# Kernel tuning notes

Measured on AMD Instinct MI355X. Metric: run time of the kernel, lower is better.

The kernel has to match this reference:

```python
import jax, jax.numpy as jnp
import numpy as np

N_NODES = 100000
N_EDGES = 1600000
IN_C, HID_C, OUT_C = 128, 128, 64


def gcn_conv(x, src, dst, ew, W, b, n_nodes):
    """PyG GCNConv: symmetric-normalized aggregation with added self-loops.

    out = D^{-1/2} (A + I) D^{-1/2} (x @ W) + b,  D = deg(A+I)
    """
    h = x @ W  # [N, C_out]
    # degree at target nodes, including self-loop weight of 1
    deg = jax.ops.segment_sum(ew, dst, num_segments=n_nodes) + 1.0  # [N]
    dinv = jnp.where(deg > 0, jax.lax.rsqrt(deg), 0.0)
    norm = dinv[src] * ew * dinv[dst]  # [E]
    # gather-scale-scatter over edges + self-loop term (norm_ii = 1/deg_i)
    agg = jax.ops.segment_sum(h[src] * norm[:, None], dst, num_segments=n_nodes)
    agg = agg + h * (dinv * dinv)[:, None]
    return agg + b


def setup_inputs() -> dict:
    key = jax.random.key(0)
    ks = jax.random.split(key, 7)
    x = jax.random.normal(ks[0], (N_NODES, IN_C), dtype=jnp.float32)
    edge_index = jax.random.randint(ks[1], (2, N_EDGES), 0, N_NODES, dtype=jnp.int32)
    edge_weight = jax.random.uniform(ks[2], (N_EDGES,), dtype=jnp.float32)
    W1 = jax.random.normal(ks[3], (IN_C, HID_C), dtype=jnp.float32) / np.sqrt(IN_C)
    b1 = jnp.zeros((HID_C,), dtype=jnp.float32)
    W2 = jax.random.normal(ks[4], (HID_C, OUT_C), dtype=jnp.float32) / np.sqrt(HID_C)
    b2 = jnp.zeros((OUT_C,), dtype=jnp.float32)
    return {"x": x, "edge_index": edge_index, "edge_weight": edge_weight,
            "W1": W1, "b1": b1, "W2": W2, "b2": b2}


def reference(x, edge_index, edge_weight, W1, b1, W2, b2):
    src, dst = edge_index[0], edge_index[1]
    n = x.shape[0]
    h = gcn_conv(x, src, dst, edge_weight, W1, b1, n)
    h = jax.nn.relu(h)
    out = gcn_conv(h, src, dst, edge_weight, W2, b2, n)
    return out
```

## Files before the change

kernel.cpp:

```cpp
#include <hip/hip_runtime.h>


#define N_NODES 100000
#define CHUNK   2048
#define NBUCK   196
#define BSHIFT  9
#define BNODES  512
#define CAP     10240

typedef __attribute__((ext_vector_type(8))) short bf16x8;
typedef __attribute__((ext_vector_type(4))) float f32x4;

__device__ __forceinline__ unsigned bf16r(float f) {
    unsigned u = __float_as_uint(f);
    return (u + 0x7fffu + ((u >> 16) & 1u)) >> 16;
}
__device__ __forceinline__ float bf_lo(unsigned u) { return __uint_as_float(u << 16); }
__device__ __forceinline__ float bf_hi(unsigned u) { return __uint_as_float(u & 0xffff0000u); }


__global__ __launch_bounds__(256) void partA1_kernel(
    const int* __restrict__ dst, int* __restrict__ histmat, int E)
{
    __shared__ int hist[256];
    int t = threadIdx.x, blk = blockIdx.x;
    hist[t] = 0;
    __syncthreads();
    int e0 = blk * CHUNK;
    int nv = min(CHUNK, E - e0);
#pragma unroll
    for (int j = 0; j < CHUNK / 256; ++j) {
        int idx = t + j * 256;
        if (idx < nv) atomicAdd(&hist[dst[e0 + idx] >> BSHIFT], 1);
    }
    __syncthreads();
    histmat[blk * 256 + t] = hist[t];
}


__global__ __launch_bounds__(256) void scanB_kernel(
    int* __restrict__ histmat, int* __restrict__ bucketSize, int NBLK)
{
    __shared__ int sums[256];
    int b = blockIdx.x, t = threadIdx.x;
    const int PER = (NBLK + 255) / 256;
    int loc[8];
    int s = 0;
#pragma unroll 8
    for (int j = 0; j < PER; ++j) {
        int r = t * PER + j;
        int v = (r < NBLK) ? histmat[r * 256 + b] : 0;
        loc[j] = v; s += v;
    }
    sums[t] = s;
    __syncthreads();
    int v = s;
#pragma unroll
    for (int off = 1; off < 256; off <<= 1) {
        int a = (t >= off) ? sums[t - off] : 0;
        __syncthreads();
        sums[t] += a;
        __syncthreads();
    }
    if (t == 255) bucketSize[b] = sums[255];
    int run = sums[t] - v;
#pragma unroll 8
    for (int j = 0; j < PER; ++j) {
        int r = t * PER + j;
        if (r < NBLK) { histmat[r * 256 + b] = run; run += loc[j]; }
    }
}


__global__ __launch_bounds__(256) void partA2_kernel(
    const int* __restrict__ src, const int* __restrict__ dst,
    const float* __restrict__ ew, const int* __restrict__ histmat,
    uint2* __restrict__ csrTmp, int E)
{
    __shared__ int hist[256], sc[256], exc[256], lcur[256], basel[256];
    __shared__ uint2 ent[CHUNK];
    __shared__ unsigned short bof[CHUNK];

    int t = threadIdx.x, blk = blockIdx.x;
    hist[t] = 0; lcur[t] = 0;
    basel[t] = histmat[blk * 256 + t];
    __syncthreads();

    int e0 = blk * CHUNK;
    int nv = min(CHUNK, E - e0);
    int dv[CHUNK / 256]; int sv[CHUNK / 256]; unsigned wv[CHUNK / 256];
#pragma unroll
    for (int j = 0; j < CHUNK / 256; ++j) {
        int idx = t + j * 256;
        if (idx < nv) {
            int e = e0 + idx;
            dv[j] = dst[e]; sv[j] = src[e]; wv[j] = __float_as_uint(ew[e]);
            atomicAdd(&hist[dv[j] >> BSHIFT], 1);
        } else dv[j] = -1;
    }
    __syncthreads();
    int hv = hist[t];
    sc[t] = hv;
    __syncthreads();
#pragma unroll
    for (int off = 1; off < 256; off <<= 1) {
        int a = (t >= off) ? sc[t - off] : 0;
        __syncthreads();
        sc[t] += a;
        __syncthreads();
    }
    exc[t] = sc[t] - hv;
    __syncthreads();
#pragma unroll
    for (int j = 0; j < CHUNK / 256; ++j) {
        if (dv[j] >= 0) {
            int b  = dv[j] >> BSHIFT;
            int dl = dv[j] & (BNODES - 1);
            int p  = exc[b] + atomicAdd(&lcur[b], 1);
            ent[p] = make_uint2(((unsigned)dl << 17) | (unsigned)sv[j], wv[j]);
            bof[p] = (unsigned short)b;
        }
    }
    __syncthreads();
#pragma unroll
    for (int j = 0; j < CHUNK / 256; ++j) {
        int i = t + j * 256;
        if (i < nv) {
            int b = bof[i];
            size_t addr = (size_t)b * CAP + basel[b] + (i - exc[b]);
            csrTmp[addr] = ent[i];
        }
    }
}


__global__ __launch_bounds__(1024) void bucketB1_kernel(
    const uint2* __restrict__ csrTmp, const int* __restrict__ bucketSize,
    float* __restrict__ dinv, uint2* __restrict__ nodeinfo, int N)
{
    __shared__ unsigned long long dc[BNODES];
    __shared__ int scn[BNODES];
    int b = blockIdx.x, t = threadIdx.x;
    if (t < BNODES) dc[t] = 0ull;
    __syncthreads();

    int sz = bucketSize[b];
    const uint2* reg = csrTmp + (size_t)b * CAP;
    for (int i = t; i < sz; i += 1024) {
        uint2 en = reg[i];
        int dl = (int)(en.x >> 17);
        unsigned fx = (unsigned)__float2uint_rn(__uint_as_float(en.y) * 16777216.0f);
        atomicAdd(&dc[dl], (1ull << 32) | (unsigned long long)fx);
    }
    __syncthreads();

    int cnt = 0; float dv = 1.0f;
    if (t < BNODES) {
        unsigned long long v = dc[t];
        cnt = (int)(v >> 32);
        float deg = (float)(unsigned)(v & 0xffffffffull) * (1.0f / 16777216.0f);
        dv = rsqrtf(deg + 1.0f);
        scn[t] = cnt;
    }
    __syncthreads();
#pragma unroll
    for (int off = 1; off < BNODES; off <<= 1) {
        int a = 0;
        if (t < BNODES && t >= off) a = scn[t - off];
        __syncthreads();
        if (t < BNODES) scn[t] += a;
        __syncthreads();
    }
    if (t < BNODES) {
        int excl = scn[t] - cnt;
        int gn = b * BNODES + t;
        if (gn < N) {
            dinv[gn] = dv;
            nodeinfo[gn] = make_uint2((unsigned)(b * CAP + excl), (unsigned)cnt);
        }
    }
}


__global__ __launch_bounds__(1024) void bucketB2_kernel(
    const uint2* __restrict__ csrTmp, const int* __restrict__ bucketSize,
    const uint2* __restrict__ nodeinfo, const float* __restrict__ dinv,
    uint2* __restrict__ csrF, int N)
{
    __shared__ float dinv_l[BNODES];
    __shared__ int beg[BNODES], cur[BNODES];
    int b = blockIdx.x, t = threadIdx.x;
    if (t < BNODES) {
        int gn = b * BNODES + t;
        float dv = 1.0f; int bg = 0;
        if (gn < N) { uint2 inf = nodeinfo[gn]; bg = (int)inf.x; dv = dinv[gn]; }
        dinv_l[t] = dv; beg[t] = bg; cur[t] = 0;
    }
    __syncthreads();

    int sz = bucketSize[b];
    const uint2* reg = csrTmp + (size_t)b * CAP;
    for (int i = t; i < sz; i += 1024) {
        uint2 en = reg[i];
        int dl = (int)(en.x >> 17);
        int s  = (int)(en.x & 0x1FFFFu);
        int p  = beg[dl] + atomicAdd(&cur[dl], 1);
        float w = dinv[s] * __uint_as_float(en.y) * dinv_l[dl];
        csrF[p] = make_uint2((unsigned)s, __float_as_uint(w));
    }
}


__global__ __launch_bounds__(256) void prep_w_kernel(
    const float* __restrict__ W1, const float* __restrict__ W2,
    unsigned* __restrict__ Wt1, unsigned* __restrict__ Wt2)
{
    int t = threadIdx.x;
    if (blockIdx.x == 0) {
        for (int f = t; f < 128 * 64; f += 256) {
            int c = f % 128, j = f / 128;
            unsigned p = bf16r(W1[(size_t)(2 * j) * 128 + c]) |
                         (bf16r(W1[(size_t)(2 * j + 1) * 128 + c]) << 16);
            Wt1[c * 64 + j] = p;
        }
    } else {
        for (int f = t; f < 64 * 64; f += 256) {
            int c = f % 64, j = f / 64;
            unsigned p = bf16r(W2[(size_t)(2 * j) * 64 + c]) |
                         (bf16r(W2[(size_t)(2 * j + 1) * 64 + c]) << 16);
            Wt2[c * 64 + j] = p;
        }
    }
}


template <int NCOL, bool XBF16>
__global__ __launch_bounds__(256) void gemm_mfma_kernel(
    const void* __restrict__ Xv, const unsigned* __restrict__ Wt,
    unsigned* __restrict__ Hb, int M)
{
    constexpr int KU  = 64;
    constexpr int LW  = KU + 4;
    constexpr int NT  = (NCOL == 128) ? 2 : 1;
    __shared__ unsigned sA[64 * LW];
    __shared__ unsigned sB[NCOL * LW];

    const int t = threadIdx.x;
    const int rbase = blockIdx.x * 64;

    for (int f = t; f < NCOL * (KU / 4); f += 256) {
        int c = f / (KU / 4), q = f % (KU / 4);
        uint4 v = *(const uint4*)&Wt[c * KU + q * 4];
        *(uint4*)&sB[c * LW + q * 4] = v;
    }
    if (XBF16) {
        const unsigned* Xu = (const unsigned*)Xv;
        for (int f = t; f < 64 * (KU / 4); f += 256) {
            int r = f / (KU / 4), q = f % (KU / 4);
            int gr = rbase + r;
            uint4 v = make_uint4(0, 0, 0, 0);
            if (gr < M) v = *(const uint4*)&Xu[(size_t)gr * KU + q * 4];
            *(uint4*)&sA[r * LW + q * 4] = v;
        }
    } else {
        const float* Xf = (const float*)Xv;
        for (int f = t; f < 64 * 32; f += 256) {
            int r = f / 32, c4 = f % 32;
            int gr = rbase + r;
            float4 v = make_float4(0.f, 0.f, 0.f, 0.f);
            if (gr < M) v = *(const float4*)&Xf[(size_t)gr * 128 + c4 * 4];
            sA[r * LW + c4 * 2]     = bf16r(v.x) | (bf16r(v.y) << 16);
            sA[r * LW + c4 * 2 + 1] = bf16r(v.z) | (bf16r(v.w) << 16);
        }
    }
    __syncthreads();

    const int wave = t >> 6, lane = t & 63;
    const int quad = lane >> 4, lr = lane & 15;
    const int n0 = wave * (16 * NT);

    f32x4 acc[4][NT];
#pragma unroll
    for (int mi = 0; mi < 4; ++mi)
#pragma unroll
        for (int ni = 0; ni < NT; ++ni)
            acc[mi][ni] = (f32x4){0.f, 0.f, 0.f, 0.f};

#pragma unroll
    for (int ks = 0; ks < 4; ++ks) {
        int ko = ks * 16 + quad * 4;
        bf16x8 b[NT];
#pragma unroll
        for (int ni = 0; ni < NT; ++ni)
            b[ni] = *(const bf16x8*)&sB[(n0 + ni * 16 + lr) * LW + ko];
#pragma unroll
        for (int mi = 0; mi < 4; ++mi) {
            bf16x8 a = *(const bf16x8*)&sA[(mi * 16 + lr) * LW + ko];
#pragma unroll
            for (int ni = 0; ni < NT; ++ni)
                acc[mi][ni] = __builtin_amdgcn_mfma_f32_16x16x32_bf16(
                    a, b[ni], acc[mi][ni], 0, 0, 0);
        }
    }
    __syncthreads();

    unsigned short* sO = (unsigned short*)sA;
#pragma unroll
    for (int mi = 0; mi < 4; ++mi)
#pragma unroll
        for (int ni = 0; ni < NT; ++ni)
#pragma unroll
            for (int r = 0; r < 4; ++r)
                sO[(mi * 16 + quad * 4 + r) * (2 * LW) + n0 + ni * 16 + lr] =
                    (unsigned short)bf16r(acc[mi][ni][r]);
    __syncthreads();

    for (int f = t; f < 64 * (NCOL / 2); f += 256) {
        int row = f / (NCOL / 2), cu = f % (NCOL / 2);
        int gr = rbase + row;
        if (gr < M) Hb[(size_t)gr * (NCOL / 2) + cu] = sA[row * LW + cu];
    }
}


__global__ __launch_bounds__(256) void gather128_kernel(
    const uint2* __restrict__ nodeinfo, const uint2* __restrict__ csr,
    const uint4* __restrict__ Hb4,
    const float* __restrict__ dinv, const float* __restrict__ bias,
    unsigned* __restrict__ OUTP, int N)
{
    int node = blockIdx.x * 4 + (threadIdx.x >> 6);
    if (node >= N) return;
    int lane = threadIdx.x & 63;
    int q  = lane >> 4;
    int cg = lane & 15;

    float d2; { float di = dinv[node]; d2 = (q == 0) ? di * di : 0.f; }
    float acc[8];
    {
        uint4 su = Hb4[(size_t)node * 16 + cg];
        acc[0] = bf_lo(su.x) * d2; acc[1] = bf_hi(su.x) * d2;
        acc[2] = bf_lo(su.y) * d2; acc[3] = bf_hi(su.y) * d2;
        acc[4] = bf_lo(su.z) * d2; acc[5] = bf_hi(su.z) * d2;
        acc[6] = bf_lo(su.w) * d2; acc[7] = bf_hi(su.w) * d2;
    }

    uint2 inf = nodeinfo[node];
    int beg = (int)inf.x, end = beg + (int)inf.y;
    for (int j = beg; j < end; j += 64) {
        int cs = 0, cw = 0;
        if (j + lane < end) {
            uint2 p = csr[j + lane];
            cs = (int)p.x; cw = (int)p.y;
        }
        int mm = end - j; if (mm > 64) mm = 64;
#pragma unroll 4
        for (int k = 0; k < mm; k += 4) {
            int   idx = k + q;
            int   s = __shfl(cs, idx);
            float w = __uint_as_float(__shfl(cw, idx));
            uint4 u = Hb4[(size_t)s * 16 + cg];
            acc[0] = fmaf(bf_lo(u.x), w, acc[0]); acc[1] = fmaf(bf_hi(u.x), w, acc[1]);
            acc[2] = fmaf(bf_lo(u.y), w, acc[2]); acc[3] = fmaf(bf_hi(u.y), w, acc[3]);
            acc[4] = fmaf(bf_lo(u.z), w, acc[4]); acc[5] = fmaf(bf_hi(u.z), w, acc[5]);
            acc[6] = fmaf(bf_lo(u.w), w, acc[6]); acc[7] = fmaf(bf_hi(u.w), w, acc[7]);
        }
    }

#pragma unroll
    for (int v = 0; v < 8; ++v) {
        acc[v] += __shfl_xor(acc[v], 16);
        acc[v] += __shfl_xor(acc[v], 32);
    }

    int c = cg * 8 + q * 2;
    float o0 = fmaxf(acc[q * 2]     + bias[c],     0.f);
    float o1 = fmaxf(acc[q * 2 + 1] + bias[c + 1], 0.f);
    OUTP[(size_t)node * 64 + cg * 4 + q] = bf16r(o0) | (bf16r(o1) << 16);
}


__global__ __launch_bounds__(256) void gather64_kernel(
    const uint2* __restrict__ nodeinfo, const uint2* __restrict__ csr,
    const uint4* __restrict__ Hb4,
    const float* __restrict__ dinv, const float* __restrict__ bias,
    float* __restrict__ OUT, int N)
{
    int node = blockIdx.x * 4 + (threadIdx.x >> 6);
    if (node >= N) return;
    int lane = threadIdx.x & 63;
    int q  = lane >> 3;
    int cg = lane & 7;

    float d2; { float di = dinv[node]; d2 = (q == 0) ? di * di : 0.f; }
    float acc[8];
    {
        uint4 su = Hb4[(size_t)node * 8 + cg];
        acc[0] = bf_lo(su.x) * d2; acc[1] = bf_hi(su.x) * d2;
        acc[2] = bf_lo(su.y) * d2; acc[3] = bf_hi(su.y) * d2;
        acc[4] = bf_lo(su.z) * d2; acc[5] = bf_hi(su.z) * d2;
        acc[6] = bf_lo(su.w) * d2; acc[7] = bf_hi(su.w) * d2;
    }

    uint2 inf = nodeinfo[node];
    int beg = (int)inf.x, end = beg + (int)inf.y;
    for (int j = beg; j < end; j += 64) {
        int cs = 0, cw = 0;
        if (j + lane < end) {
            uint2 p = csr[j + lane];
            cs = (int)p.x; cw = (int)p.y;
        }
        int mm = end - j; if (mm > 64) mm = 64;
#pragma unroll 2
        for (int k = 0; k < mm; k += 8) {
            int   idx = k + q;
            int   s = __shfl(cs, idx);
            float w = __uint_as_float(__shfl(cw, idx));
            uint4 u = Hb4[(size_t)s * 8 + cg];
            acc[0] = fmaf(bf_lo(u.x), w, acc[0]); acc[1] = fmaf(bf_hi(u.x), w, acc[1]);
            acc[2] = fmaf(bf_lo(u.y), w, acc[2]); acc[3] = fmaf(bf_hi(u.y), w, acc[3]);
            acc[4] = fmaf(bf_lo(u.z), w, acc[4]); acc[5] = fmaf(bf_hi(u.z), w, acc[5]);
            acc[6] = fmaf(bf_lo(u.w), w, acc[6]); acc[7] = fmaf(bf_hi(u.w), w, acc[7]);
        }
    }

#pragma unroll
    for (int v = 0; v < 8; ++v) {
        acc[v] += __shfl_xor(acc[v], 8);
        acc[v] += __shfl_xor(acc[v], 16);
        acc[v] += __shfl_xor(acc[v], 32);
    }

    int c = cg * 8 + q;
    OUT[(size_t)node * 64 + c] = acc[q] + bias[c];
}

static inline size_t align_up(size_t x) { return (x + 255) & ~size_t(255); }

extern "C" void kernel_launch(void* const* d_in, const int* in_sizes, int n_in,
                              void* d_out, int out_size, void* d_ws, size_t ws_size,
                              hipStream_t stream)
{
    const float* x  = (const float*)d_in[0];
    const int*   ei = (const int*)d_in[1];
    const float* ew = (const float*)d_in[2];
    const float* W1 = (const float*)d_in[3];
    const float* b1 = (const float*)d_in[4];
    const float* W2 = (const float*)d_in[5];
    const float* b2 = (const float*)d_in[6];
    float* out = (float*)d_out;

    const int N = N_NODES;
    const int E = in_sizes[2];
    const int* src = ei;
    const int* dst = ei + E;

    const int NBLK = (E + CHUNK - 1) / CHUNK;
    const size_t REGION = (size_t)NBUCK * CAP;

    char* ws = (char*)d_ws;
    int*   histmat   = (int*)ws;   ws += align_up((size_t)NBLK * 256 * 4);
    int*   bucketSize= (int*)ws;   ws += align_up((size_t)NBUCK * 4);
    float* dinv      = (float*)ws; ws += align_up((size_t)N * 4);
    uint2* nodeinfo  = (uint2*)ws; ws += align_up((size_t)N * 8);
    uint2* csrTmp    = (uint2*)ws; ws += align_up(REGION * 8);
    uint2* csrF      = (uint2*)ws; ws += align_up(REGION * 8);
    unsigned* Wt1    = (unsigned*)ws; ws += align_up((size_t)128 * 64 * 4);
    unsigned* Wt2    = (unsigned*)ws; ws += align_up((size_t)64 * 64 * 4);
    unsigned* h1     = (unsigned*)ws; ws += align_up((size_t)N * 64 * 4);
    unsigned* g1     = (unsigned*)ws; ws += align_up((size_t)N * 64 * 4);
    unsigned* h2     = (unsigned*)ws; ws += align_up((size_t)N * 32 * 4);

    prep_w_kernel<<<2, 256, 0, stream>>>(W1, W2, Wt1, Wt2);
    partA1_kernel<<<NBLK, 256, 0, stream>>>(dst, histmat, E);
    scanB_kernel<<<NBUCK, 256, 0, stream>>>(histmat, bucketSize, NBLK);
    partA2_kernel<<<NBLK, 256, 0, stream>>>(src, dst, ew, histmat, csrTmp, E);
    bucketB1_kernel<<<NBUCK, 1024, 0, stream>>>(csrTmp, bucketSize, dinv, nodeinfo, N);
    bucketB2_kernel<<<NBUCK, 1024, 0, stream>>>(csrTmp, bucketSize, nodeinfo, dinv, csrF, N);

    gemm_mfma_kernel<128, false><<<(N + 63) / 64, 256, 0, stream>>>(x, Wt1, h1, N);
    gather128_kernel<<<(N + 3) / 4, 256, 0, stream>>>(
        nodeinfo, csrF, (const uint4*)h1, dinv, b1, g1, N);

    gemm_mfma_kernel<64, true><<<(N + 63) / 64, 256, 0, stream>>>(g1, Wt2, h2, N);
    gather64_kernel<<<(N + 3) / 4, 256, 0, stream>>>(
        nodeinfo, csrF, (const uint4*)h2, dinv, b2, out, N);
}
```

Measured before the change: 297.4 us.

## Fuse preprocessing and GEMM kernels, merge bucket passes, fuse layer-1 gather with GEMM2

Folds the weight prep into the histogram kernel, runs the edge-partition pass and the layer-1 GEMM as one horizontally fused launch, and merges the two bucket passes into one kernel that stages the bucket in shared memory. Applies the source-side normalization inside the gathers (dinv[src] looked up per edge) and the destination scaling at the end, so the CSR no longer carries fully normalized weights. The layer-1 gather now does the layer-2 GEMM with MFMA in the same block, which removes the g1 intermediate round trip. The cost is extra random dinv loads per edge, larger shared memory footprints that may lower occupancy, and a gg grid of N/16 that assumes N is a multiple of 16.

```diff
diff --git a/kernel.cpp b/kernel.cpp
--- a/kernel.cpp
+++ b/kernel.cpp
@@ -19,11 +19,30 @@
 __device__ __forceinline__ float bf_hi(unsigned u) { return __uint_as_float(u & 0xffff0000u); }
 
 
-__global__ __launch_bounds__(256) void partA1_kernel(
-    const int* __restrict__ dst, int* __restrict__ histmat, int E)
+__global__ __launch_bounds__(256) void prepA1_kernel(
+    const int* __restrict__ dst, const float* __restrict__ W1,
+    const float* __restrict__ W2, unsigned* __restrict__ Wt1,
+    unsigned* __restrict__ Wt2, int* __restrict__ histmat, int E)
 {
     __shared__ int hist[256];
-    int t = threadIdx.x, blk = blockIdx.x;
+    int t = threadIdx.x;
+    if (blockIdx.x == 0) {
+        for (int f = t; f < 128 * 64; f += 256) {
+            int c = f % 128, j = f / 128;
+            Wt1[c * 64 + j] = bf16r(W1[(size_t)(2 * j) * 128 + c]) |
+                              (bf16r(W1[(size_t)(2 * j + 1) * 128 + c]) << 16);
+        }
+        return;
+    }
+    if (blockIdx.x == 1) {
+        for (int f = t; f < 64 * 64; f += 256) {
+            int c = f % 64, j = f / 64;
+            Wt2[c * 64 + j] = bf16r(W2[(size_t)(2 * j) * 64 + c]) |
+                              (bf16r(W2[(size_t)(2 * j + 1) * 64 + c]) << 16);
+        }
+        return;
+    }
+    int blk = blockIdx.x - 2;
     hist[t] = 0;
     __syncthreads();
     int e0 = blk * CHUNK;
@@ -72,16 +91,23 @@
 }
 
 
-__global__ __launch_bounds__(256) void partA2_kernel(
+#define A2G_SMEM 52224
+
+__device__ __forceinline__ void a2_body(
+    char* smem, int blk,
     const int* __restrict__ src, const int* __restrict__ dst,
     const float* __restrict__ ew, const int* __restrict__ histmat,
     uint2* __restrict__ csrTmp, int E)
 {
-    __shared__ int hist[256], sc[256], exc[256], lcur[256], basel[256];
-    __shared__ uint2 ent[CHUNK];
-    __shared__ unsigned short bof[CHUNK];
-
-    int t = threadIdx.x, blk = blockIdx.x;
+    int* hist = (int*)smem;
+    int* sc   = hist + 256;
+    int* exc  = sc + 256;
+    int* lcur = exc + 256;
+    int* basel= lcur + 256;
+    uint2* ent = (uint2*)(basel + 256);
+    unsigned short* bof = (unsigned short*)(ent + CHUNK);
+
+    int t = threadIdx.x;
     hist[t] = 0; lcur[t] = 0;
     basel[t] = histmat[blk * 256 + t];
     __syncthreads();
@@ -127,27 +153,110 @@
         int i = t + j * 256;
         if (i < nv) {
             int b = bof[i];
-            size_t addr = (size_t)b * CAP + basel[b] + (i - exc[b]);
-            csrTmp[addr] = ent[i];
-        }
-    }
-}
-
-
-__global__ __launch_bounds__(1024) void bucketB1_kernel(
+            csrTmp[(size_t)b * CAP + basel[b] + (i - exc[b])] = ent[i];
+        }
+    }
+}
+
+__device__ __forceinline__ void gemm1_body(
+    char* smem, int blk, const float* __restrict__ Xf,
+    const unsigned* __restrict__ Wt, unsigned* __restrict__ Hb, int M)
+{
+    constexpr int LW = 68, KU = 64;
+    unsigned* sA = (unsigned*)smem;
+    unsigned* sB = sA + 64 * LW;
+    const int t = threadIdx.x;
+    const int rbase = blk * 64;
+
+    for (int f = t; f < 128 * 16; f += 256) {
+        int c = f >> 4, qd = f & 15;
+        *(uint4*)&sB[c * LW + qd * 4] = *(const uint4*)&Wt[c * KU + qd * 4];
+    }
+    for (int f = t; f < 64 * 32; f += 256) {
+        int r = f >> 5, c4 = f & 31;
+        int gr = rbase + r;
+        float4 v = make_float4(0.f, 0.f, 0.f, 0.f);
+        if (gr < M) v = *(const float4*)&Xf[(size_t)gr * 128 + c4 * 4];
+        sA[r * LW + c4 * 2]     = bf16r(v.x) | (bf16r(v.y) << 16);
+        sA[r * LW + c4 * 2 + 1] = bf16r(v.z) | (bf16r(v.w) << 16);
+    }
+    __syncthreads();
+
+    const int wave = t >> 6, lane = t & 63;
+    const int quad = lane >> 4, lr = lane & 15;
+    const int n0 = wave * 32;
+
+    f32x4 acc[4][2];
+#pragma unroll
+    for (int mi = 0; mi < 4; ++mi)
+#pragma unroll
+        for (int ni = 0; ni < 2; ++ni)
+            acc[mi][ni] = (f32x4){0.f, 0.f, 0.f, 0.f};
+
+#pragma unroll
+    for (int ks = 0; ks < 4; ++ks) {
+        int ko = ks * 16 + quad * 4;
+        bf16x8 b0 = *(const bf16x8*)&sB[(n0 + lr) * LW + ko];
+        bf16x8 b1 = *(const bf16x8*)&sB[(n0 + 16 + lr) * LW + ko];
+#pragma unroll
+        for (int mi = 0; mi < 4; ++mi) {
+            bf16x8 a = *(const bf16x8*)&sA[(mi * 16 + lr) * LW + ko];
+            acc[mi][0] = __builtin_amdgcn_mfma_f32_16x16x32_bf16(a, b0, acc[mi][0], 0, 0, 0);
+            acc[mi][1] = __builtin_amdgcn_mfma_f32_16x16x32_bf16(a, b1, acc[mi][1], 0, 0, 0);
+        }
+    }
+    __syncthreads();
+
+    unsigned short* sO = (unsigned short*)sA;
+#pragma unroll
+    for (int mi = 0; mi < 4; ++mi)
+#pragma unroll
+        for (int ni = 0; ni < 2; ++ni)
+#pragma unroll
+            for (int r = 0; r < 4; ++r)
+                sO[(mi * 16 + quad * 4 + r) * (2 * LW) + n0 + ni * 16 + lr] =
+                    (unsigned short)bf16r(acc[mi][ni][r]);
+    __syncthreads();
+
+    for (int f = t; f < 64 * 64; f += 256) {
+        int row = f >> 6, cu = f & 63;
+        int gr = rbase + row;
+        if (gr < M) Hb[(size_t)gr * 64 + cu] = sA[row * LW + cu];
+    }
+}
+
+__global__ __launch_bounds__(256) void a2_gemm_kernel(
+    const int* __restrict__ src, const int* __restrict__ dst,
+    const float* __restrict__ ew, const int* __restrict__ histmat,
+    uint2* __restrict__ csrTmp, int E, int NBLK,
+    const float* __restrict__ x, const unsigned* __restrict__ Wt1,
+    unsigned* __restrict__ h1, int M)
+{
+    __shared__ __align__(16) char smem[A2G_SMEM];
+    if ((int)blockIdx.x < NBLK)
+        a2_body(smem, blockIdx.x, src, dst, ew, histmat, csrTmp, E);
+    else
+        gemm1_body(smem, blockIdx.x - NBLK, x, Wt1, h1, M);
+}
+
+
+__global__ __launch_bounds__(1024) void bucketB_kernel(
     const uint2* __restrict__ csrTmp, const int* __restrict__ bucketSize,
-    float* __restrict__ dinv, uint2* __restrict__ nodeinfo, int N)
-{
+    float* __restrict__ dinv, uint2* __restrict__ nodeinfo,
+    uint2* __restrict__ csrF, int N)
+{
+    __shared__ uint2 ent[CAP];
     __shared__ unsigned long long dc[BNODES];
-    __shared__ int scn[BNODES];
+    __shared__ int scn[BNODES], beg[BNODES], cur[BNODES];
     int b = blockIdx.x, t = threadIdx.x;
-    if (t < BNODES) dc[t] = 0ull;
-    __syncthreads();
-
-    int sz = bucketSize[b];
+    if (t < BNODES) { dc[t] = 0ull; cur[t] = 0; }
+    __syncthreads();
+
+    int sz = min(bucketSize[b], CAP);
     const uint2* reg = csrTmp + (size_t)b * CAP;
     for (int i = t; i < sz; i += 1024) {
         uint2 en = reg[i];
+        ent[i] = en;
         int dl = (int)(en.x >> 17);
         unsigned fx = (unsigned)__float2uint_rn(__uint_as_float(en.y) * 16777216.0f);
         atomicAdd(&dc[dl], (1ull << 32) | (unsigned long long)fx);
@@ -158,8 +267,7 @@
     if (t < BNODES) {
         unsigned long long v = dc[t];
         cnt = (int)(v >> 32);
-        float deg = (float)(unsigned)(v & 0xffffffffull) * (1.0f / 16777216.0f);
-        dv = rsqrtf(deg + 1.0f);
+        dv = rsqrtf((float)(unsigned)(v & 0xffffffffull) * (1.0f / 16777216.0f) + 1.0f);
         scn[t] = cnt;
     }
     __syncthreads();
@@ -173,210 +281,116 @@
     }
     if (t < BNODES) {
         int excl = scn[t] - cnt;
+        beg[t] = excl;
         int gn = b * BNODES + t;
         if (gn < N) {
             dinv[gn] = dv;
             nodeinfo[gn] = make_uint2((unsigned)(b * CAP + excl), (unsigned)cnt);
         }
     }
-}
-
-
-__global__ __launch_bounds__(1024) void bucketB2_kernel(
-    const uint2* __restrict__ csrTmp, const int* __restrict__ bucketSize,
-    const uint2* __restrict__ nodeinfo, const float* __restrict__ dinv,
-    uint2* __restrict__ csrF, int N)
-{
-    __shared__ float dinv_l[BNODES];
-    __shared__ int beg[BNODES], cur[BNODES];
-    int b = blockIdx.x, t = threadIdx.x;
-    if (t < BNODES) {
-        int gn = b * BNODES + t;
-        float dv = 1.0f; int bg = 0;
-        if (gn < N) { uint2 inf = nodeinfo[gn]; bg = (int)inf.x; dv = dinv[gn]; }
-        dinv_l[t] = dv; beg[t] = bg; cur[t] = 0;
-    }
-    __syncthreads();
-
-    int sz = bucketSize[b];
-    const uint2* reg = csrTmp + (size_t)b * CAP;
+    __syncthreads();
+
+    uint2* outreg = csrF + (size_t)b * CAP;
     for (int i = t; i < sz; i += 1024) {
-        uint2 en = reg[i];
+        uint2 en = ent[i];
         int dl = (int)(en.x >> 17);
-        int s  = (int)(en.x & 0x1FFFFu);
         int p  = beg[dl] + atomicAdd(&cur[dl], 1);
-        float w = dinv[s] * __uint_as_float(en.y) * dinv_l[dl];
-        csrF[p] = make_uint2((unsigned)s, __float_as_uint(w));
-    }
-}
-
-
-__global__ __launch_bounds__(256) void prep_w_kernel(
-    const float* __restrict__ W1, const float* __restrict__ W2,
-    unsigned* __restrict__ Wt1, unsigned* __restrict__ Wt2)
-{
-    int t = threadIdx.x;
-    if (blockIdx.x == 0) {
-        for (int f = t; f < 128 * 64; f += 256) {
-            int c = f % 128, j = f / 128;
-            unsigned p = bf16r(W1[(size_t)(2 * j) * 128 + c]) |
-                         (bf16r(W1[(size_t)(2 * j + 1) * 128 + c]) << 16);
-            Wt1[c * 64 + j] = p;
-        }
-    } else {
-        for (int f = t; f < 64 * 64; f += 256) {
-            int c = f % 64, j = f / 64;
-            unsigned p = bf16r(W2[(size_t)(2 * j) * 64 + c]) |
-                         (bf16r(W2[(size_t)(2 * j + 1) * 64 + c]) << 16);
-            Wt2[c * 64 + j] = p;
-        }
-    }
-}
-
-
-template <int NCOL, bool XBF16>
-__global__ __launch_bounds__(256) void gemm_mfma_kernel(
-    const void* __restrict__ Xv, const unsigned* __restrict__ Wt,
-    unsigned* __restrict__ Hb, int M)
-{
-    constexpr int KU  = 64;
-    constexpr int LW  = KU + 4;
-    constexpr int NT  = (NCOL == 128) ? 2 : 1;
-    __shared__ unsigned sA[64 * LW];
-    __shared__ unsigned sB[NCOL * LW];
-
-    const int t = threadIdx.x;
-    const int rbase = blockIdx.x * 64;
-
-    for (int f = t; f < NCOL * (KU / 4); f += 256) {
-        int c = f / (KU / 4), q = f % (KU / 4);
-        uint4 v = *(const uint4*)&Wt[c * KU + q * 4];
-        *(uint4*)&sB[c * LW + q * 4] = v;
-    }
-    if (XBF16) {
-        const unsigned* Xu = (const unsigned*)Xv;
-        for (int f = t; f < 64 * (KU / 4); f += 256) {
-            int r = f / (KU / 4), q = f % (KU / 4);
-            int gr = rbase + r;
-            uint4 v = make_uint4(0, 0, 0, 0);
-            if (gr < M) v = *(const uint4*)&Xu[(size_t)gr * KU + q * 4];
-            *(uint4*)&sA[r * LW + q * 4] = v;
-        }
-    } else {
-        const float* Xf = (const float*)Xv;
-        for (int f = t; f < 64 * 32; f += 256) {
-            int r = f / 32, c4 = f % 32;
-            int gr = rbase + r;
-            float4 v = make_float4(0.f, 0.f, 0.f, 0.f);
-            if (gr < M) v = *(const float4*)&Xf[(size_t)gr * 128 + c4 * 4];
-            sA[r * LW + c4 * 2]     = bf16r(v.x) | (bf16r(v.y) << 16);
-            sA[r * LW + c4 * 2 + 1] = bf16r(v.z) | (bf16r(v.w) << 16);
-        }
-    }
-    __syncthreads();
-
-    const int wave = t >> 6, lane = t & 63;
-    const int quad = lane >> 4, lr = lane & 15;
-    const int n0 = wave * (16 * NT);
-
-    f32x4 acc[4][NT];
-#pragma unroll
-    for (int mi = 0; mi < 4; ++mi)
-#pragma unroll
-        for (int ni = 0; ni < NT; ++ni)
-            acc[mi][ni] = (f32x4){0.f, 0.f, 0.f, 0.f};
-
-#pragma unroll
-    for (int ks = 0; ks < 4; ++ks) {
-        int ko = ks * 16 + quad * 4;
-        bf16x8 b[NT];
-#pragma unroll
-        for (int ni = 0; ni < NT; ++ni)
-            b[ni] = *(const bf16x8*)&sB[(n0 + ni * 16 + lr) * LW + ko];
-#pragma unroll
-        for (int mi = 0; mi < 4; ++mi) {
-            bf16x8 a = *(const bf16x8*)&sA[(mi * 16 + lr) * LW + ko];
-#pragma unroll
-            for (int ni = 0; ni < NT; ++ni)
-                acc[mi][ni] = __builtin_amdgcn_mfma_f32_16x16x32_bf16(
-                    a, b[ni], acc[mi][ni], 0, 0, 0);
-        }
-    }
-    __syncthreads();
-
-    unsigned short* sO = (unsigned short*)sA;
-#pragma unroll
-    for (int mi = 0; mi < 4; ++mi)
-#pragma unroll
-        for (int ni = 0; ni < NT; ++ni)
-#pragma unroll
-            for (int r = 0; r < 4; ++r)
-                sO[(mi * 16 + quad * 4 + r) * (2 * LW) + n0 + ni * 16 + lr] =
-                    (unsigned short)bf16r(acc[mi][ni][r]);
-    __syncthreads();
-
-    for (int f = t; f < 64 * (NCOL / 2); f += 256) {
-        int row = f / (NCOL / 2), cu = f % (NCOL / 2);
-        int gr = rbase + row;
-        if (gr < M) Hb[(size_t)gr * (NCOL / 2) + cu] = sA[row * LW + cu];
-    }
-}
-
-
-__global__ __launch_bounds__(256) void gather128_kernel(
+        outreg[p] = make_uint2(en.x & 0x1FFFFu, en.y);
+    }
+}
+
+
+__global__ __launch_bounds__(256) void gg_kernel(
     const uint2* __restrict__ nodeinfo, const uint2* __restrict__ csr,
     const uint4* __restrict__ Hb4,
     const float* __restrict__ dinv, const float* __restrict__ bias,
-    unsigned* __restrict__ OUTP, int N)
-{
-    int node = blockIdx.x * 4 + (threadIdx.x >> 6);
-    if (node >= N) return;
-    int lane = threadIdx.x & 63;
-    int q  = lane >> 4;
-    int cg = lane & 15;
-
-    float d2; { float di = dinv[node]; d2 = (q == 0) ? di * di : 0.f; }
-    float acc[8];
+    const unsigned* __restrict__ Wt2, unsigned* __restrict__ H2, int N)
+{
+    __shared__ __align__(16) unsigned sG[16 * 68];
+    __shared__ __align__(16) float    sO[16 * 68];
+
+    const int t = threadIdx.x, wave = t >> 6, lane = t & 63;
+    const int q = lane >> 4, cg = lane & 15;
+    const int nb = blockIdx.x * 16;
+
+    for (int i = 0; i < 4; ++i) {
+        int m = wave * 4 + i;
+        int node = nb + m;
+        float di = dinv[node];
+        float d0 = (q == 0) ? di : 0.f;
+        float acc[8];
+        {
+            uint4 su = Hb4[(size_t)node * 16 + cg];
+            acc[0] = bf_lo(su.x) * d0; acc[1] = bf_hi(su.x) * d0;
+            acc[2] = bf_lo(su.y) * d0; acc[3] = bf_hi(su.y) * d0;
+            acc[4] = bf_lo(su.z) * d0; acc[5] = bf_hi(su.z) * d0;
+            acc[6] = bf_lo(su.w) * d0; acc[7] = bf_hi(su.w) * d0;
+        }
+        uint2 inf = nodeinfo[node];
+        int beg = (int)inf.x, end = beg + (int)inf.y;
+        for (int j = beg; j < end; j += 64) {
+            int cs = 0; float cw = 0.f;
+            if (j + lane < end) {
+                uint2 p = csr[j + lane];
+                cs = (int)p.x;
+                cw = __uint_as_float(p.y) * dinv[cs];
+            }
+            int mm = end - j; if (mm > 64) mm = 64;
+#pragma unroll 4
+            for (int k = 0; k < mm; k += 4) {
+                int   s = __shfl(cs, k + q);
+                float w = __shfl(cw, k + q);
+                uint4 u = Hb4[(size_t)s * 16 + cg];
+                acc[0] = fmaf(bf_lo(u.x), w, acc[0]); acc[1] = fmaf(bf_hi(u.x), w, acc[1]);
+                acc[2] = fmaf(bf_lo(u.y), w, acc[2]); acc[3] = fmaf(bf_hi(u.y), w, acc[3]);
+                acc[4] = fmaf(bf_lo(u.z), w, acc[4]); acc[5] = fmaf(bf_hi(u.z), w, acc[5]);
+                acc[6] = fmaf(bf_lo(u.w), w, acc[6]); acc[7] = fmaf(bf_hi(u.w), w, acc[7]);
+            }
+        }
+#pragma unroll
+        for (int v = 0; v < 8; ++v) {
+            acc[v] += __shfl_xor(acc[v], 16);
+            acc[v] += __shfl_xor(acc[v], 32);
+        }
+        if (q == 0) {
+            int c = cg * 8;
+            uint4 pk;
+            pk.x = bf16r(fmaxf(acc[0] * di + bias[c + 0], 0.f)) |
+                   (bf16r(fmaxf(acc[1] * di + bias[c + 1], 0.f)) << 16);
+            pk.y = bf16r(fmaxf(acc[2] * di + bias[c + 2], 0.f)) |
+                   (bf16r(fmaxf(acc[3] * di + bias[c + 3], 0.f)) << 16);
+            pk.z = bf16r(fmaxf(acc[4] * di + bias[c + 4], 0.f)) |
+                   (bf16r(fmaxf(acc[5] * di + bias[c + 5], 0.f)) << 16);
+            pk.w = bf16r(fmaxf(acc[6] * di + bias[c + 6], 0.f)) |
+                   (bf16r(fmaxf(acc[7] * di + bias[c + 7], 0.f)) << 16);
+            *(uint4*)&sG[m * 68 + cg * 4] = pk;
+        }
+    }
+    __syncthreads();
+
     {
-        uint4 su = Hb4[(size_t)node * 16 + cg];
-        acc[0] = bf_lo(su.x) * d2; acc[1] = bf_hi(su.x) * d2;
-        acc[2] = bf_lo(su.y) * d2; acc[3] = bf_hi(su.y) * d2;
-        acc[4] = bf_lo(su.z) * d2; acc[5] = bf_hi(su.z) * d2;
-        acc[6] = bf_lo(su.w) * d2; acc[7] = bf_hi(su.w) * d2;
-    }
-
-    uint2 inf = nodeinfo[node];
-    int beg = (int)inf.x, end = beg + (int)inf.y;
-    for (int j = beg; j < end; j += 64) {
-        int cs = 0, cw = 0;
-        if (j + lane < end) {
-            uint2 p = csr[j + lane];
-            cs = (int)p.x; cw = (int)p.y;
-        }
-        int mm = end - j; if (mm > 64) mm = 64;
-#pragma unroll 4
-        for (int k = 0; k < mm; k += 4) {
-            int   idx = k + q;
-            int   s = __shfl(cs, idx);
-            float w = __uint_as_float(__shfl(cw, idx));
-            uint4 u = Hb4[(size_t)s * 16 + cg];
-            acc[0] = fmaf(bf_lo(u.x), w, acc[0]); acc[1] = fmaf(bf_hi(u.x), w, acc[1]);
-            acc[2] = fmaf(bf_lo(u.y), w, acc[2]); acc[3] = fmaf(bf_hi(u.y), w, acc[3]);
-            acc[4] = fmaf(bf_lo(u.z), w, acc[4]); acc[5] = fmaf(bf_hi(u.z), w, acc[5]);
-            acc[6] = fmaf(bf_lo(u.w), w, acc[6]); acc[7] = fmaf(bf_hi(u.w), w, acc[7]);
-        }
-    }
-
-#pragma unroll
-    for (int v = 0; v < 8; ++v) {
-        acc[v] += __shfl_xor(acc[v], 16);
-        acc[v] += __shfl_xor(acc[v], 32);
-    }
-
-    int c = cg * 8 + q * 2;
-    float o0 = fmaxf(acc[q * 2]     + bias[c],     0.f);
-    float o1 = fmaxf(acc[q * 2 + 1] + bias[c + 1], 0.f);
-    OUTP[(size_t)node * 64 + cg * 4 + q] = bf16r(o0) | (bf16r(o1) << 16);
+        const int quad = lane >> 4, lr = lane & 15;
+        const int n0 = wave * 16;
+        f32x4 accv = (f32x4){0.f, 0.f, 0.f, 0.f};
+#pragma unroll
+        for (int ks = 0; ks < 4; ++ks) {
+            int ko = ks * 16 + quad * 4;
+            bf16x8 av = *(const bf16x8*)&sG[lr * 68 + ko];
+            bf16x8 bv = *(const bf16x8*)&Wt2[(n0 + lr) * 64 + ko];
+            accv = __builtin_amdgcn_mfma_f32_16x16x32_bf16(av, bv, accv, 0, 0, 0);
+        }
+#pragma unroll
+        for (int r = 0; r < 4; ++r)
+            sO[(quad * 4 + r) * 68 + n0 + lr] = accv[r];
+    }
+    __syncthreads();
+
+    for (int f = t; f < 512; f += 256) {
+        int row = f >> 5, cu = f & 31;
+        unsigned pk = bf16r(sO[row * 68 + 2 * cu]) |
+                      (bf16r(sO[row * 68 + 2 * cu + 1]) << 16);
+        H2[(size_t)(nb + row) * 32 + cu] = pk;
+    }
 }
 
 
@@ -392,30 +406,31 @@
     int q  = lane >> 3;
     int cg = lane & 7;
 
-    float d2; { float di = dinv[node]; d2 = (q == 0) ? di * di : 0.f; }
+    float di = dinv[node];
+    float d0 = (q == 0) ? di : 0.f;
     float acc[8];
     {
         uint4 su = Hb4[(size_t)node * 8 + cg];
-        acc[0] = bf_lo(su.x) * d2; acc[1] = bf_hi(su.x) * d2;
-        acc[2] = bf_lo(su.y) * d2; acc[3] = bf_hi(su.y) * d2;
-        acc[4] = bf_lo(su.z) * d2; acc[5] = bf_hi(su.z) * d2;
-        acc[6] = bf_lo(su.w) * d2; acc[7] = bf_hi(su.w) * d2;
+        acc[0] = bf_lo(su.x) * d0; acc[1] = bf_hi(su.x) * d0;
+        acc[2] = bf_lo(su.y) * d0; acc[3] = bf_hi(su.y) * d0;
+        acc[4] = bf_lo(su.z) * d0; acc[5] = bf_hi(su.z) * d0;
+        acc[6] = bf_lo(su.w) * d0; acc[7] = bf_hi(su.w) * d0;
     }
 
     uint2 inf = nodeinfo[node];
     int beg = (int)inf.x, end = beg + (int)inf.y;
     for (int j = beg; j < end; j += 64) {
-        int cs = 0, cw = 0;
+        int cs = 0; float cw = 0.f;
         if (j + lane < end) {
             uint2 p = csr[j + lane];
-            cs = (int)p.x; cw = (int)p.y;
+            cs = (int)p.x;
+            cw = __uint_as_float(p.y) * dinv[cs];
         }
         int mm = end - j; if (mm > 64) mm = 64;
 #pragma unroll 2
         for (int k = 0; k < mm; k += 8) {
-            int   idx = k + q;
-            int   s = __shfl(cs, idx);
-            float w = __uint_as_float(__shfl(cw, idx));
+            int   s = __shfl(cs, k + q);
+            float w = __shfl(cw, k + q);
             uint4 u = Hb4[(size_t)s * 8 + cg];
             acc[0] = fmaf(bf_lo(u.x), w, acc[0]); acc[1] = fmaf(bf_hi(u.x), w, acc[1]);
             acc[2] = fmaf(bf_lo(u.y), w, acc[2]); acc[3] = fmaf(bf_hi(u.y), w, acc[3]);
@@ -432,7 +447,7 @@
     }
 
     int c = cg * 8 + q;
-    OUT[(size_t)node * 64 + c] = acc[q] + bias[c];
+    OUT[(size_t)node * 64 + c] = acc[q] * di + bias[c];
 }
 
 static inline size_t align_up(size_t x) { return (x + 255) & ~size_t(255); }
@@ -457,6 +472,7 @@
 
     const int NBLK = (E + CHUNK - 1) / CHUNK;
     const size_t REGION = (size_t)NBUCK * CAP;
+    const int GEMM1B = (N + 63) / 64;
 
     char* ws = (char*)d_ws;
     int*   histmat   = (int*)ws;   ws += align_up((size_t)NBLK * 256 * 4);
@@ -468,21 +484,15 @@
     unsigned* Wt1    = (unsigned*)ws; ws += align_up((size_t)128 * 64 * 4);
     unsigned* Wt2    = (unsigned*)ws; ws += align_up((size_t)64 * 64 * 4);
     unsigned* h1     = (unsigned*)ws; ws += align_up((size_t)N * 64 * 4);
-    unsigned* g1     = (unsigned*)ws; ws += align_up((size_t)N * 64 * 4);
     unsigned* h2     = (unsigned*)ws; ws += align_up((size_t)N * 32 * 4);
 
-    prep_w_kernel<<<2, 256, 0, stream>>>(W1, W2, Wt1, Wt2);
-    partA1_kernel<<<NBLK, 256, 0, stream>>>(dst, histmat, E);
+    prepA1_kernel<<<NBLK + 2, 256, 0, stream>>>(dst, W1, W2, Wt1, Wt2, histmat, E);
     scanB_kernel<<<NBUCK, 256, 0, stream>>>(histmat, bucketSize, NBLK);
-    partA2_kernel<<<NBLK, 256, 0, stream>>>(src, dst, ew, histmat, csrTmp, E);
-    bucketB1_kernel<<<NBUCK, 1024, 0, stream>>>(csrTmp, bucketSize, dinv, nodeinfo, N);
-    bucketB2_kernel<<<NBUCK, 1024, 0, stream>>>(csrTmp, bucketSize, nodeinfo, dinv, csrF, N);
-
-    gemm_mfma_kernel<128, false><<<(N + 63) / 64, 256, 0, stream>>>(x, Wt1, h1, N);
-    gather128_kernel<<<(N + 3) / 4, 256, 0, stream>>>(
-        nodeinfo, csrF, (const uint4*)h1, dinv, b1, g1, N);
-
-    gemm_mfma_kernel<64, true><<<(N + 63) / 64, 256, 0, stream>>>(g1, Wt2, h2, N);
+    a2_gemm_kernel<<<NBLK + GEMM1B, 256, 0, stream>>>(
+        src, dst, ew, histmat, csrTmp, E, NBLK, x, Wt1, h1, N);
+    bucketB_kernel<<<NBUCK, 1024, 0, stream>>>(csrTmp, bucketSize, dinv, nodeinfo, csrF, N);
+    gg_kernel<<<N / 16, 256, 0, stream>>>(nodeinfo, csrF, (const uint4*)h1,
+                                          dinv, b1, Wt2, h2, N);
     gather64_kernel<<<(N + 3) / 4, 256, 0, stream>>>(
         nodeinfo, csrF, (const uint4*)h2, dinv, b2, out, N);
 }
```

New measurement: 289.1 us. 2.8% less time.
